# Kernel optimization log

Measured on AMD Instinct MI355X. Metric: run time of the kernel, lower is better.

The kernel has to match this reference:

```python
import jax, jax.numpy as jnp
import numpy as np

H = 1024   # hidden_size
V = 16000  # output_size (vocab)
B = 64     # batch_size
L = 256    # max_length (encoder seq len)
T = 128    # decoder steps


def setup_inputs() -> dict:
    key = jax.random.key(0)
    ks = jax.random.split(key, 16)
    s = 0.02
    return {
        "target_inputs": jax.random.randint(ks[0], (B, T), 0, V, dtype=jnp.int64),
        "encoder_outputs": jax.random.normal(ks[1], (L, B, H), dtype=jnp.float32),
        "emb": jax.random.normal(ks[2], (V, H), dtype=jnp.float32) * s,
        "W_attn": jax.random.normal(ks[3], (L, 2 * H), dtype=jnp.float32) * s,
        "b_attn": jnp.zeros((L,), jnp.float32),
        "W_comb": jax.random.normal(ks[4], (H, 2 * H), dtype=jnp.float32) * s,
        "b_comb": jnp.zeros((H,), jnp.float32),
        "W_ih": jax.random.normal(ks[5], (4 * H, H), dtype=jnp.float32) * s,
        "W_hh": jax.random.normal(ks[6], (4 * H, H), dtype=jnp.float32) * s,
        "b_ih": jnp.zeros((4 * H,), jnp.float32),
        "b_hh": jnp.zeros((4 * H,), jnp.float32),
        "W_out": jax.random.normal(ks[7], (V, H), dtype=jnp.float32) * s,
        "b_out": jnp.zeros((V,), jnp.float32),
    }


def reference(target_inputs, encoder_outputs, emb, W_attn, b_attn, W_comb, b_comb,
              W_ih, W_hh, b_ih, b_hh, W_out, b_out):
    dec_h = encoder_outputs[-1]                      # [B,H] (dec_hid.squeeze(0))
    enc = jnp.transpose(encoder_outputs, (1, 0, 2))  # [B,L,H]
    dec_c = jnp.zeros_like(dec_h)
    tokens = target_inputs.T                         # [T,B]

    def step(carry, tok):
        h, c = carry
        e = emb[tok]                                              # [B,H]  (dropout = eval identity)
        scores = jnp.concatenate([e, h], 1) @ W_attn.T + b_attn  # [B,L]
        aw = jax.nn.softmax(scores, axis=1)
        ctx = jnp.einsum('bl,blh->bh', aw, enc)                  # bmm
        x = jnp.concatenate([e, ctx], 1) @ W_comb.T + b_comb
        x = jax.nn.relu(x)                                        # [B,H]
        # single-step LSTM (PyTorch gate order i,f,g,o)
        gates = x @ W_ih.T + b_ih + h @ W_hh.T + b_hh             # [B,4H]
        i, f, g, o = jnp.split(gates, 4, axis=1)
        c = jax.nn.sigmoid(f) * c + jax.nn.sigmoid(i) * jnp.tanh(g)
        h = jax.nn.sigmoid(o) * jnp.tanh(c)
        logits = h @ W_out.T + b_out                              # [B,V]
        # Faithful to original: F.log_softmax(out(output_i.squeeze(1)), dim=1)
        # where output_i is [1,B,V]; squeeze(1) is a no-op for B>1, so dim=1
        # normalizes over the BATCH axis (== axis 0 of [B,V] here).
        out = jax.nn.log_softmax(logits, axis=0)
        return (h, c), out

    (_, _), outs = jax.lax.scan(step, (dec_h, dec_c), tokens)
    return outs  # [T,B,V]
```

## Files before the change

### kernel.cpp

```cpp
#include <hip/hip_runtime.h>
#include <math.h>

#define HH 1024
#define VV 16000
#define BB 64
#define LL 256
#define TT 128


__device__ __forceinline__ float sigm(float x) { return 1.0f / (1.0f + expf(-x)); }

__device__ void lstm_apply(const float* __restrict__ gates_acc,
                           const float* __restrict__ b_ih,
                           const float* __restrict__ b_hh,
                           float* __restrict__ c_buf,
                           float* __restrict__ h_buf,
                           float* __restrict__ Hall_t,
                           float* h_s,
                           int b, int tid, bool first_c)
{
    const int j = tid * 4;
    const float* gb = gates_acc + (size_t)b * 4 * HH;
    float4 gi = *(const float4*)(gb + j);
    float4 gf = *(const float4*)(gb + HH + j);
    float4 gg = *(const float4*)(gb + 2 * HH + j);
    float4 go = *(const float4*)(gb + 3 * HH + j);
    float4 bii = *(const float4*)(b_ih + j),          bhi = *(const float4*)(b_hh + j);
    float4 bif_ = *(const float4*)(b_ih + HH + j),    bhf = *(const float4*)(b_hh + HH + j);
    float4 big = *(const float4*)(b_ih + 2 * HH + j), bhg = *(const float4*)(b_hh + 2 * HH + j);
    float4 bio = *(const float4*)(b_ih + 3 * HH + j), bho = *(const float4*)(b_hh + 3 * HH + j);
    float4 co = first_c ? make_float4(0.f, 0.f, 0.f, 0.f)
                        : *(const float4*)(c_buf + (size_t)b * HH + j);
    float4 cn, hn;
#define DO_LSTM(X)                                        \
    {                                                     \
        float iv = sigm(gi.X + bii.X + bhi.X);            \
        float fv = sigm(gf.X + bif_.X + bhf.X);           \
        float gv = tanhf(gg.X + big.X + bhg.X);           \
        float ov = sigm(go.X + bio.X + bho.X);            \
        float c2 = fv * co.X + iv * gv;                   \
        cn.X = c2;                                        \
        hn.X = ov * tanhf(c2);                            \
    }
    DO_LSTM(x) DO_LSTM(y) DO_LSTM(z) DO_LSTM(w)
#undef DO_LSTM
    *(float4*)(c_buf + (size_t)b * HH + j) = cn;
    *(float4*)(h_buf + (size_t)b * HH + j) = hn;
    *(float4*)(Hall_t + (size_t)b * HH + j) = hn;
    if (h_s) *(float4*)(h_s + j) = hn;
}

__global__ __launch_bounds__(256) void k_attn(
    const int* __restrict__ tok_all, const float* __restrict__ enc,
    const float* __restrict__ emb, const float* __restrict__ Wattn,
    const float* __restrict__ battn, const float* __restrict__ b_ih,
    const float* __restrict__ b_hh, float* __restrict__ Hall,
    float* __restrict__ xin, float* __restrict__ x_acc,
    const float* __restrict__ gates_acc, float* __restrict__ h_buf,
    float* __restrict__ c_buf, int t)
{
    const int b = blockIdx.x;
    const int tid = threadIdx.x;
    __shared__ float e_s[HH];
    __shared__ float h_s[HH];
    __shared__ float sc[LL];
    __shared__ float red[8];

    ((float4*)(x_acc + (size_t)b * HH))[tid] = make_float4(0.f, 0.f, 0.f, 0.f);

    const int is64 = (tok_all[1] == 0 && tok_all[3] == 0 && tok_all[5] == 0 && tok_all[7] == 0);
    const int tok = is64 ? tok_all[2 * (b * TT + t)] : tok_all[b * TT + t];

    float4 ev = ((const float4*)(emb + (size_t)tok * HH))[tid];
    ((float4*)e_s)[tid] = ev;
    ((float4*)(xin + (size_t)b * 2 * HH))[tid] = ev;

    if (t == 0) {
        float4 hv = ((const float4*)(enc + (size_t)(LL - 1) * BB * HH + (size_t)b * HH))[tid];
        ((float4*)h_s)[tid] = hv;
        ((float4*)(h_buf + (size_t)b * HH))[tid] = hv;
    } else {
        lstm_apply(gates_acc, b_ih, b_hh, c_buf, h_buf,
                   Hall + (size_t)(t - 1) * BB * HH, h_s, b, tid, t == 1);
    }
    __syncthreads();

    const int w = tid >> 6, lane = tid & 63;
    const float4* es4 = (const float4*)e_s;
    const float4* hs4 = (const float4*)h_s;
    for (int li = 0; li < 64; ++li) {
        const int l = w * 64 + li;
        const float4* wr = (const float4*)(Wattn + (size_t)l * 2 * HH);
        float a = 0.f;
#pragma unroll
        for (int it = 0; it < 4; ++it) {
            float4 wv = wr[it * 64 + lane];
            float4 xv = es4[it * 64 + lane];
            a += wv.x * xv.x + wv.y * xv.y + wv.z * xv.z + wv.w * xv.w;
        }
#pragma unroll
        for (int it = 0; it < 4; ++it) {
            float4 wv = wr[256 + it * 64 + lane];
            float4 xv = hs4[it * 64 + lane];
            a += wv.x * xv.x + wv.y * xv.y + wv.z * xv.z + wv.w * xv.w;
        }
#pragma unroll
        for (int o = 32; o > 0; o >>= 1) a += __shfl_down(a, o, 64);
        if (lane == 0) sc[l] = a + battn[l];
    }
    __syncthreads();

    const float sv = sc[tid];
    float m = sv;
#pragma unroll
    for (int o = 32; o > 0; o >>= 1) m = fmaxf(m, __shfl_down(m, o, 64));
    if (lane == 0) red[w] = m;
    __syncthreads();
    m = fmaxf(fmaxf(red[0], red[1]), fmaxf(red[2], red[3]));
    const float ex = expf(sv - m);
    float s = ex;
#pragma unroll
    for (int o = 32; o > 0; o >>= 1) s += __shfl_down(s, o, 64);
    if (lane == 0) red[4 + w] = s;
    __syncthreads();
    const float tot = red[4] + red[5] + red[6] + red[7];
    sc[tid] = ex / tot;
    __syncthreads();

    float4 ctx = make_float4(0.f, 0.f, 0.f, 0.f);
    const float4* ebase = (const float4*)(enc + (size_t)b * HH) + tid;
#pragma unroll 4
    for (int l = 0; l < LL; ++l) {
        const float a = sc[l];
        float4 e2 = ebase[(size_t)l * (BB * HH / 4)];
        ctx.x += a * e2.x; ctx.y += a * e2.y; ctx.z += a * e2.z; ctx.w += a * e2.w;
    }
    ((float4*)(xin + (size_t)b * 2 * HH + HH))[tid] = ctx;
}

template <bool RELU_BIAS>
__device__ void gemm64x64(const float* __restrict__ A, int lda,
                          const float* __restrict__ abias,
                          const float* __restrict__ Wm, int ldw,
                          int n0, int k0, int klen,
                          float* __restrict__ Cacc, int ldc)
{
    __shared__ float As[32][68];
    __shared__ float Ws[32][68];
    const int tid = threadIdx.x;
    const int ty = tid >> 4, tx = tid & 15;
    const int q = tid & 7, r = tid >> 3;
    float acc[4][4] = {};

    for (int kc = k0; kc < k0 + klen; kc += 32) {
#pragma unroll
        for (int rr = 0; rr < 2; ++rr) {
            const int row = r + rr * 32;
            float4 v = *(const float4*)(A + (size_t)row * lda + kc + q * 4);
            if (RELU_BIAS) {
                const float4 bv = *(const float4*)(abias + kc + q * 4);
                v.x = fmaxf(v.x + bv.x, 0.f);
                v.y = fmaxf(v.y + bv.y, 0.f);
                v.z = fmaxf(v.z + bv.z, 0.f);
                v.w = fmaxf(v.w + bv.w, 0.f);
            }
            As[q * 4 + 0][row] = v.x; As[q * 4 + 1][row] = v.y;
            As[q * 4 + 2][row] = v.z; As[q * 4 + 3][row] = v.w;
            float4 wv = *(const float4*)(Wm + (size_t)(n0 + row) * ldw + kc + q * 4);
            Ws[q * 4 + 0][row] = wv.x; Ws[q * 4 + 1][row] = wv.y;
            Ws[q * 4 + 2][row] = wv.z; Ws[q * 4 + 3][row] = wv.w;
        }
        __syncthreads();
#pragma unroll
        for (int k = 0; k < 32; ++k) {
            const float4 a = *(const float4*)&As[k][ty * 4];
            const float4 wv = *(const float4*)&Ws[k][tx * 4];
            const float av[4] = {a.x, a.y, a.z, a.w};
            const float bv[4] = {wv.x, wv.y, wv.z, wv.w};
#pragma unroll
            for (int i = 0; i < 4; ++i)
#pragma unroll
                for (int j = 0; j < 4; ++j) acc[i][j] += av[i] * bv[j];
        }
        __syncthreads();
    }
#pragma unroll
    for (int i = 0; i < 4; ++i)
#pragma unroll
        for (int j = 0; j < 4; ++j)
            atomicAdd(Cacc + (size_t)(ty * 4 + i) * ldc + n0 + tx * 4 + j, acc[i][j]);
}

__global__ __launch_bounds__(256) void k_comb(const float* __restrict__ xin,
                                              const float* __restrict__ Wcomb,
                                              float* __restrict__ x_acc,
                                              float* __restrict__ gates_acc)
{
    const int blin = blockIdx.y * gridDim.x + blockIdx.x;
    float4* gz = (float4*)gates_acc;
    gz[blin * 512 + threadIdx.x] = make_float4(0.f, 0.f, 0.f, 0.f);
    gz[blin * 512 + 256 + threadIdx.x] = make_float4(0.f, 0.f, 0.f, 0.f);
    gemm64x64<false>(xin, 2 * HH, nullptr, Wcomb, 2 * HH,
                     blockIdx.x * 64, blockIdx.y * 256, 256, x_acc, HH);
}

__global__ __launch_bounds__(256) void k_gates(const float* __restrict__ x_acc,
                                               const float* __restrict__ h_buf,
                                               const float* __restrict__ b_comb,
                                               const float* __restrict__ W_ih,
                                               const float* __restrict__ W_hh,
                                               float* __restrict__ gates_acc)
{
    const int n0 = blockIdx.x * 64;
    const int k0 = blockIdx.y * 512;
    if (k0 < HH)
        gemm64x64<true>(x_acc, HH, b_comb, W_ih, HH, n0, k0, 512, gates_acc, 4 * HH);
    else
        gemm64x64<false>(h_buf, HH, nullptr, W_hh, HH, n0, k0 - HH, 512, gates_acc, 4 * HH);
}

__global__ __launch_bounds__(256) void k_lstm_fin(const float* __restrict__ gates_acc,
                                                  const float* __restrict__ b_ih,
                                                  const float* __restrict__ b_hh,
                                                  float* __restrict__ c_buf,
                                                  float* __restrict__ h_buf,
                                                  float* __restrict__ Hall)
{
    lstm_apply(gates_acc, b_ih, b_hh, c_buf, h_buf,
               Hall + (size_t)(TT - 1) * BB * HH, nullptr, blockIdx.x, threadIdx.x, false);
}

__global__ __launch_bounds__(256) void k_out(const float* __restrict__ Hall,
                                             const float* __restrict__ Wout,
                                             float* __restrict__ out)
{
    const int t = blockIdx.y;
    const int n0 = blockIdx.x * 128;
    const float* A = Hall + (size_t)t * BB * HH;
    __shared__ float As[32][68];
    __shared__ float Ws[32][132];
    __shared__ float Cs[64][129];
    __shared__ float lse_s[128];
    const int tid = threadIdx.x;
    const int ty = tid >> 4, tx = tid & 15;
    const int q = tid & 7, r = tid >> 3;
    float acc[4][8] = {};

    for (int kc = 0; kc < HH; kc += 32) {
#pragma unroll
        for (int rr = 0; rr < 2; ++rr) {
            const int row = r + rr * 32;
            float4 v = *(const float4*)(A + (size_t)row * HH + kc + q * 4);
            As[q * 4 + 0][row] = v.x; As[q * 4 + 1][row] = v.y;
            As[q * 4 + 2][row] = v.z; As[q * 4 + 3][row] = v.w;
        }
#pragma unroll
        for (int rr = 0; rr < 4; ++rr) {
            const int row = r + rr * 32;
            float4 v = *(const float4*)(Wout + (size_t)(n0 + row) * HH + kc + q * 4);
            Ws[q * 4 + 0][row] = v.x; Ws[q * 4 + 1][row] = v.y;
            Ws[q * 4 + 2][row] = v.z; Ws[q * 4 + 3][row] = v.w;
        }
        __syncthreads();
#pragma unroll
        for (int k = 0; k < 32; ++k) {
            const float4 a = *(const float4*)&As[k][ty * 4];
            const float4 w0 = *(const float4*)&Ws[k][tx * 8];
            const float4 w1 = *(const float4*)&Ws[k][tx * 8 + 4];
            const float av[4] = {a.x, a.y, a.z, a.w};
            const float bv[8] = {w0.x, w0.y, w0.z, w0.w, w1.x, w1.y, w1.z, w1.w};
#pragma unroll
            for (int i = 0; i < 4; ++i)
#pragma unroll
                for (int j = 0; j < 8; ++j) acc[i][j] += av[i] * bv[j];
        }
        __syncthreads();
    }
#pragma unroll
    for (int i = 0; i < 4; ++i)
#pragma unroll
        for (int j = 0; j < 8; ++j) Cs[ty * 4 + i][tx * 8 + j] = acc[i][j];
    __syncthreads();

    if (tid < 128) {
        float m = -1e30f;
        for (int b = 0; b < 64; ++b) m = fmaxf(m, Cs[b][tid]);
        float s = 0.f;
        for (int b = 0; b < 64; ++b) s += expf(Cs[b][tid] - m);
        lse_s[tid] = m + logf(s);
    }
    __syncthreads();

    const int col = tid & 127, bh = tid >> 7;
    float* outp = out + (size_t)t * BB * VV + n0 + col;
    for (int b = bh; b < 64; b += 2)
        outp[(size_t)b * VV] = Cs[b][col] - lse_s[col];
}

extern "C" void kernel_launch(void* const* d_in, const int* in_sizes, int n_in,
                              void* d_out, int out_size, void* d_ws, size_t ws_size,
                              hipStream_t stream)
{
    const int* tok = (const int*)d_in[0];
    const float* enc = (const float*)d_in[1];
    const float* emb = (const float*)d_in[2];
    const float* W_attn = (const float*)d_in[3];
    const float* b_attn = (const float*)d_in[4];
    const float* W_comb = (const float*)d_in[5];
    const float* b_comb = (const float*)d_in[6];
    const float* W_ih = (const float*)d_in[7];
    const float* W_hh = (const float*)d_in[8];
    const float* b_ih = (const float*)d_in[9];
    const float* b_hh = (const float*)d_in[10];
    const float* W_out = (const float*)d_in[11];
    float* out = (float*)d_out;
    float* ws = (float*)d_ws;

    const size_t n_Hall = (size_t)TT * BB * HH;
    const size_t n_xin = (size_t)BB * 2 * HH;
    const size_t n_xacc = (size_t)BB * HH;
    const size_t n_gates = (size_t)BB * 4 * HH;
    const size_t needed = (n_Hall + n_xin + n_xacc + n_gates + 2 * (size_t)BB * HH) * 4;
    if (ws_size < needed) return;

    float* H_all = ws;
    float* xin = H_all + n_Hall;
    float* x_acc = xin + n_xin;
    float* gates_acc = x_acc + n_xacc;
    float* h_buf = gates_acc + n_gates;
    float* c_buf = h_buf + (size_t)BB * HH;

    for (int t = 0; t < TT; ++t) {
        k_attn<<<BB, 256, 0, stream>>>(tok, enc, emb, W_attn, b_attn, b_ih, b_hh,
                                       H_all, xin, x_acc, gates_acc, h_buf, c_buf, t);
        k_comb<<<dim3(16, 8), 256, 0, stream>>>(xin, W_comb, x_acc, gates_acc);
        k_gates<<<dim3(64, 4), 256, 0, stream>>>(x_acc, h_buf, b_comb, W_ih, W_hh,
                                                 gates_acc);
    }
    k_lstm_fin<<<BB, 256, 0, stream>>>(gates_acc, b_ih, b_hh, c_buf, h_buf, H_all);
    k_out<<<dim3(125, 128), 256, 0, stream>>>(H_all, W_out, out);
}
```

Measured before the change: 31.68 ms.

## Fuse decoder time loop into one persistent kernel with grid barriers

Replaces the three kernel launches per decoder step with a single persistent 256-block kernel. It synchronises phases with a hierarchical atomic grid barrier and splits attention scores and context across four blocks per batch row to raise parallelism. The LSTM cell state is double-buffered so that redundant per-block LSTM recomputation can read old state safely. Register prefetching of the next K-tile is also added to the GEMM tiles and the output projection. The persistent design removes launch overhead but relies on all 256 blocks being co-resident, and the barriers add their own spin-wait cost.

```diff
diff --git a/kernel.cpp b/kernel.cpp
--- a/kernel.cpp
+++ b/kernel.cpp
@@ -7,17 +7,51 @@
 #define LL 256
 #define TT 128
 
+#define NBLK 256
+
+
+__device__ __forceinline__ void grid_barrier(unsigned* bar)
+{
+    __syncthreads();
+    if (threadIdx.x == 0) {
+        __threadfence();
+        unsigned* gen = bar;
+        unsigned* gcnt = bar + 64 + (blockIdx.x >> 4) * 64;
+        unsigned* root = bar + 1536;
+        const unsigned g =
+            __hip_atomic_load(gen, __ATOMIC_RELAXED, __HIP_MEMORY_SCOPE_AGENT);
+        bool releaser = false;
+        if (__hip_atomic_fetch_add(gcnt, 1u, __ATOMIC_ACQ_REL,
+                                   __HIP_MEMORY_SCOPE_AGENT) == 15u) {
+            __hip_atomic_store(gcnt, 0u, __ATOMIC_RELAXED,
+                               __HIP_MEMORY_SCOPE_AGENT);
+            if (__hip_atomic_fetch_add(root, 1u, __ATOMIC_ACQ_REL,
+                                       __HIP_MEMORY_SCOPE_AGENT) == 15u) {
+                __hip_atomic_store(root, 0u, __ATOMIC_RELAXED,
+                                   __HIP_MEMORY_SCOPE_AGENT);
+                __hip_atomic_store(gen, g + 1u, __ATOMIC_RELEASE,
+                                   __HIP_MEMORY_SCOPE_AGENT);
+                releaser = true;
+            }
+        }
+        if (!releaser) {
+            while (__hip_atomic_load(gen, __ATOMIC_ACQUIRE,
+                                     __HIP_MEMORY_SCOPE_AGENT) == g)
+                __builtin_amdgcn_s_sleep(1);
+        }
+        __threadfence();
+    }
+    __syncthreads();
+}
 
 __device__ __forceinline__ float sigm(float x) { return 1.0f / (1.0f + expf(-x)); }
 
-__device__ void lstm_apply(const float* __restrict__ gates_acc,
-                           const float* __restrict__ b_ih,
-                           const float* __restrict__ b_hh,
-                           float* __restrict__ c_buf,
-                           float* __restrict__ h_buf,
-                           float* __restrict__ Hall_t,
-                           float* h_s,
-                           int b, int tid, bool first_c)
+__device__ __forceinline__ void lstm_full(
+    const float* __restrict__ gates_acc, const float* __restrict__ b_ih,
+    const float* __restrict__ b_hh, const float* __restrict__ c_rd,
+    float* __restrict__ c_wr, float* __restrict__ h_buf,
+    float* __restrict__ Hall_t, float* h_s, int b, int tid, bool first_c,
+    bool writer)
 {
     const int j = tid * 4;
     const float* gb = gates_acc + (size_t)b * 4 * HH;
@@ -30,7 +64,7 @@
     float4 big = *(const float4*)(b_ih + 2 * HH + j), bhg = *(const float4*)(b_hh + 2 * HH + j);
     float4 bio = *(const float4*)(b_ih + 3 * HH + j), bho = *(const float4*)(b_hh + 3 * HH + j);
     float4 co = first_c ? make_float4(0.f, 0.f, 0.f, 0.f)
-                        : *(const float4*)(c_buf + (size_t)b * HH + j);
+                        : *(const float4*)(c_rd + (size_t)b * HH + j);
     float4 cn, hn;
 #define DO_LSTM(X)                                        \
     {                                                     \
@@ -44,133 +78,61 @@
     }
     DO_LSTM(x) DO_LSTM(y) DO_LSTM(z) DO_LSTM(w)
 #undef DO_LSTM
-    *(float4*)(c_buf + (size_t)b * HH + j) = cn;
-    *(float4*)(h_buf + (size_t)b * HH + j) = hn;
-    *(float4*)(Hall_t + (size_t)b * HH + j) = hn;
+    if (writer) {
+        *(float4*)(c_wr + (size_t)b * HH + j) = cn;
+        *(float4*)(h_buf + (size_t)b * HH + j) = hn;
+        *(float4*)(Hall_t + (size_t)b * HH + j) = hn;
+    }
     if (h_s) *(float4*)(h_s + j) = hn;
 }
 
-__global__ __launch_bounds__(256) void k_attn(
-    const int* __restrict__ tok_all, const float* __restrict__ enc,
-    const float* __restrict__ emb, const float* __restrict__ Wattn,
-    const float* __restrict__ battn, const float* __restrict__ b_ih,
-    const float* __restrict__ b_hh, float* __restrict__ Hall,
-    float* __restrict__ xin, float* __restrict__ x_acc,
-    const float* __restrict__ gates_acc, float* __restrict__ h_buf,
-    float* __restrict__ c_buf, int t)
-{
-    const int b = blockIdx.x;
-    const int tid = threadIdx.x;
-    __shared__ float e_s[HH];
-    __shared__ float h_s[HH];
-    __shared__ float sc[LL];
-    __shared__ float red[8];
-
-    ((float4*)(x_acc + (size_t)b * HH))[tid] = make_float4(0.f, 0.f, 0.f, 0.f);
-
-    const int is64 = (tok_all[1] == 0 && tok_all[3] == 0 && tok_all[5] == 0 && tok_all[7] == 0);
-    const int tok = is64 ? tok_all[2 * (b * TT + t)] : tok_all[b * TT + t];
-
-    float4 ev = ((const float4*)(emb + (size_t)tok * HH))[tid];
-    ((float4*)e_s)[tid] = ev;
-    ((float4*)(xin + (size_t)b * 2 * HH))[tid] = ev;
-
-    if (t == 0) {
-        float4 hv = ((const float4*)(enc + (size_t)(LL - 1) * BB * HH + (size_t)b * HH))[tid];
-        ((float4*)h_s)[tid] = hv;
-        ((float4*)(h_buf + (size_t)b * HH))[tid] = hv;
-    } else {
-        lstm_apply(gates_acc, b_ih, b_hh, c_buf, h_buf,
-                   Hall + (size_t)(t - 1) * BB * HH, h_s, b, tid, t == 1);
-    }
-    __syncthreads();
-
-    const int w = tid >> 6, lane = tid & 63;
-    const float4* es4 = (const float4*)e_s;
-    const float4* hs4 = (const float4*)h_s;
-    for (int li = 0; li < 64; ++li) {
-        const int l = w * 64 + li;
-        const float4* wr = (const float4*)(Wattn + (size_t)l * 2 * HH);
-        float a = 0.f;
-#pragma unroll
-        for (int it = 0; it < 4; ++it) {
-            float4 wv = wr[it * 64 + lane];
-            float4 xv = es4[it * 64 + lane];
-            a += wv.x * xv.x + wv.y * xv.y + wv.z * xv.z + wv.w * xv.w;
-        }
-#pragma unroll
-        for (int it = 0; it < 4; ++it) {
-            float4 wv = wr[256 + it * 64 + lane];
-            float4 xv = hs4[it * 64 + lane];
-            a += wv.x * xv.x + wv.y * xv.y + wv.z * xv.z + wv.w * xv.w;
-        }
-#pragma unroll
-        for (int o = 32; o > 0; o >>= 1) a += __shfl_down(a, o, 64);
-        if (lane == 0) sc[l] = a + battn[l];
-    }
-    __syncthreads();
-
-    const float sv = sc[tid];
-    float m = sv;
-#pragma unroll
-    for (int o = 32; o > 0; o >>= 1) m = fmaxf(m, __shfl_down(m, o, 64));
-    if (lane == 0) red[w] = m;
-    __syncthreads();
-    m = fmaxf(fmaxf(red[0], red[1]), fmaxf(red[2], red[3]));
-    const float ex = expf(sv - m);
-    float s = ex;
-#pragma unroll
-    for (int o = 32; o > 0; o >>= 1) s += __shfl_down(s, o, 64);
-    if (lane == 0) red[4 + w] = s;
-    __syncthreads();
-    const float tot = red[4] + red[5] + red[6] + red[7];
-    sc[tid] = ex / tot;
-    __syncthreads();
-
-    float4 ctx = make_float4(0.f, 0.f, 0.f, 0.f);
-    const float4* ebase = (const float4*)(enc + (size_t)b * HH) + tid;
-#pragma unroll 4
-    for (int l = 0; l < LL; ++l) {
-        const float a = sc[l];
-        float4 e2 = ebase[(size_t)l * (BB * HH / 4)];
-        ctx.x += a * e2.x; ctx.y += a * e2.y; ctx.z += a * e2.z; ctx.w += a * e2.w;
-    }
-    ((float4*)(xin + (size_t)b * 2 * HH + HH))[tid] = ctx;
-}
-
 template <bool RELU_BIAS>
-__device__ void gemm64x64(const float* __restrict__ A, int lda,
-                          const float* __restrict__ abias,
-                          const float* __restrict__ Wm, int ldw,
-                          int n0, int k0, int klen,
-                          float* __restrict__ Cacc, int ldc)
-{
-    __shared__ float As[32][68];
-    __shared__ float Ws[32][68];
+__device__ __forceinline__ void gemm64x64(
+    const float* __restrict__ A, int lda, const float* __restrict__ abias,
+    const float* __restrict__ Wm, int ldw, int n0, int k0, int klen,
+    float* __restrict__ Cacc, int ldc, float* __restrict__ smem)
+{
+    float (*As)[68] = (float (*)[68])smem;
+    float (*Ws)[68] = (float (*)[68])(smem + 32 * 68);
     const int tid = threadIdx.x;
     const int ty = tid >> 4, tx = tid & 15;
     const int q = tid & 7, r = tid >> 3;
     float acc[4][4] = {};
 
+    float4 va0, va1, vw0, vw1, vb;
+    {
+        const int kk = k0 + q * 4;
+        va0 = *(const float4*)(A + (size_t)r * lda + kk);
+        va1 = *(const float4*)(A + (size_t)(r + 32) * lda + kk);
+        vw0 = *(const float4*)(Wm + (size_t)(n0 + r) * ldw + kk);
+        vw1 = *(const float4*)(Wm + (size_t)(n0 + r + 32) * ldw + kk);
+        if (RELU_BIAS) vb = *(const float4*)(abias + kk);
+    }
     for (int kc = k0; kc < k0 + klen; kc += 32) {
-#pragma unroll
-        for (int rr = 0; rr < 2; ++rr) {
-            const int row = r + rr * 32;
-            float4 v = *(const float4*)(A + (size_t)row * lda + kc + q * 4);
-            if (RELU_BIAS) {
-                const float4 bv = *(const float4*)(abias + kc + q * 4);
-                v.x = fmaxf(v.x + bv.x, 0.f);
-                v.y = fmaxf(v.y + bv.y, 0.f);
-                v.z = fmaxf(v.z + bv.z, 0.f);
-                v.w = fmaxf(v.w + bv.w, 0.f);
-            }
-            As[q * 4 + 0][row] = v.x; As[q * 4 + 1][row] = v.y;
-            As[q * 4 + 2][row] = v.z; As[q * 4 + 3][row] = v.w;
-            float4 wv = *(const float4*)(Wm + (size_t)(n0 + row) * ldw + kc + q * 4);
-            Ws[q * 4 + 0][row] = wv.x; Ws[q * 4 + 1][row] = wv.y;
-            Ws[q * 4 + 2][row] = wv.z; Ws[q * 4 + 3][row] = wv.w;
-        }
+        float4 a0 = va0, a1 = va1;
+        if (RELU_BIAS) {
+            a0.x = fmaxf(a0.x + vb.x, 0.f); a0.y = fmaxf(a0.y + vb.y, 0.f);
+            a0.z = fmaxf(a0.z + vb.z, 0.f); a0.w = fmaxf(a0.w + vb.w, 0.f);
+            a1.x = fmaxf(a1.x + vb.x, 0.f); a1.y = fmaxf(a1.y + vb.y, 0.f);
+            a1.z = fmaxf(a1.z + vb.z, 0.f); a1.w = fmaxf(a1.w + vb.w, 0.f);
+        }
+        As[q * 4 + 0][r] = a0.x; As[q * 4 + 1][r] = a0.y;
+        As[q * 4 + 2][r] = a0.z; As[q * 4 + 3][r] = a0.w;
+        As[q * 4 + 0][r + 32] = a1.x; As[q * 4 + 1][r + 32] = a1.y;
+        As[q * 4 + 2][r + 32] = a1.z; As[q * 4 + 3][r + 32] = a1.w;
+        Ws[q * 4 + 0][r] = vw0.x; Ws[q * 4 + 1][r] = vw0.y;
+        Ws[q * 4 + 2][r] = vw0.z; Ws[q * 4 + 3][r] = vw0.w;
+        Ws[q * 4 + 0][r + 32] = vw1.x; Ws[q * 4 + 1][r + 32] = vw1.y;
+        Ws[q * 4 + 2][r + 32] = vw1.z; Ws[q * 4 + 3][r + 32] = vw1.w;
         __syncthreads();
+        if (kc + 32 < k0 + klen) {
+            const int kk = kc + 32 + q * 4;
+            va0 = *(const float4*)(A + (size_t)r * lda + kk);
+            va1 = *(const float4*)(A + (size_t)(r + 32) * lda + kk);
+            vw0 = *(const float4*)(Wm + (size_t)(n0 + r) * ldw + kk);
+            vw1 = *(const float4*)(Wm + (size_t)(n0 + r + 32) * ldw + kk);
+            if (RELU_BIAS) vb = *(const float4*)(abias + kk);
+        }
 #pragma unroll
         for (int k = 0; k < 32; ++k) {
             const float4 a = *(const float4*)&As[k][ty * 4];
@@ -191,43 +153,160 @@
             atomicAdd(Cacc + (size_t)(ty * 4 + i) * ldc + n0 + tx * 4 + j, acc[i][j]);
 }
 
-__global__ __launch_bounds__(256) void k_comb(const float* __restrict__ xin,
-                                              const float* __restrict__ Wcomb,
-                                              float* __restrict__ x_acc,
-                                              float* __restrict__ gates_acc)
-{
-    const int blin = blockIdx.y * gridDim.x + blockIdx.x;
-    float4* gz = (float4*)gates_acc;
-    gz[blin * 512 + threadIdx.x] = make_float4(0.f, 0.f, 0.f, 0.f);
-    gz[blin * 512 + 256 + threadIdx.x] = make_float4(0.f, 0.f, 0.f, 0.f);
-    gemm64x64<false>(xin, 2 * HH, nullptr, Wcomb, 2 * HH,
-                     blockIdx.x * 64, blockIdx.y * 256, 256, x_acc, HH);
-}
-
-__global__ __launch_bounds__(256) void k_gates(const float* __restrict__ x_acc,
-                                               const float* __restrict__ h_buf,
-                                               const float* __restrict__ b_comb,
-                                               const float* __restrict__ W_ih,
-                                               const float* __restrict__ W_hh,
-                                               float* __restrict__ gates_acc)
-{
-    const int n0 = blockIdx.x * 64;
-    const int k0 = blockIdx.y * 512;
-    if (k0 < HH)
-        gemm64x64<true>(x_acc, HH, b_comb, W_ih, HH, n0, k0, 512, gates_acc, 4 * HH);
-    else
-        gemm64x64<false>(h_buf, HH, nullptr, W_hh, HH, n0, k0 - HH, 512, gates_acc, 4 * HH);
-}
-
-__global__ __launch_bounds__(256) void k_lstm_fin(const float* __restrict__ gates_acc,
-                                                  const float* __restrict__ b_ih,
-                                                  const float* __restrict__ b_hh,
-                                                  float* __restrict__ c_buf,
-                                                  float* __restrict__ h_buf,
-                                                  float* __restrict__ Hall)
-{
-    lstm_apply(gates_acc, b_ih, b_hh, c_buf, h_buf,
-               Hall + (size_t)(TT - 1) * BB * HH, nullptr, blockIdx.x, threadIdx.x, false);
+__global__ __launch_bounds__(256) void k_loop(
+    const int* __restrict__ tok_all, const float* __restrict__ enc,
+    const float* __restrict__ emb, const float* __restrict__ Wattn,
+    const float* __restrict__ battn, const float* __restrict__ Wcomb,
+    const float* __restrict__ bcomb, const float* __restrict__ Wih,
+    const float* __restrict__ Whh, const float* __restrict__ b_ih,
+    const float* __restrict__ b_hh, float* __restrict__ Hall,
+    float* __restrict__ xin, float* __restrict__ x_acc,
+    float* __restrict__ gates_acc, float* __restrict__ h_buf,
+    float* __restrict__ c0, float* __restrict__ c1,
+    float* __restrict__ sc_all, unsigned* __restrict__ bar)
+{
+    __shared__ __align__(16) float smem[2 * 32 * 68];
+    const int bid = blockIdx.x;
+    const int tid = threadIdx.x;
+    const int w = tid >> 6, lane = tid & 63;
+
+    const int is64 = (tok_all[1] == 0 && tok_all[3] == 0 && tok_all[5] == 0 &&
+                      tok_all[7] == 0);
+
+    for (int t = 0; t < TT; ++t) {
+        {
+            const int b = bid >> 2, q = bid & 3;
+            float* e_s = smem;
+            float* h_s = smem + HH;
+
+            x_acc[(size_t)b * HH + q * 256 + tid] = 0.f;
+
+            const int tok = is64 ? tok_all[2 * (b * TT + t)] : tok_all[b * TT + t];
+            float4 ev = ((const float4*)(emb + (size_t)tok * HH))[tid];
+            ((float4*)e_s)[tid] = ev;
+            if (q == 0) ((float4*)(xin + (size_t)b * 2 * HH))[tid] = ev;
+
+            if (t == 0) {
+                float4 hv = ((const float4*)(enc + (size_t)(LL - 1) * BB * HH +
+                                             (size_t)b * HH))[tid];
+                ((float4*)h_s)[tid] = hv;
+                if (q == 0) ((float4*)(h_buf + (size_t)b * HH))[tid] = hv;
+            } else {
+                lstm_full(gates_acc, b_ih, b_hh, (t & 1) ? c1 : c0,
+                          (t & 1) ? c0 : c1, h_buf,
+                          Hall + (size_t)(t - 1) * BB * HH, h_s, b, tid,
+                          t == 1, q == 0);
+            }
+            __syncthreads();
+
+            const float4* es4 = (const float4*)e_s;
+            const float4* hs4 = (const float4*)h_s;
+            for (int i = 0; i < 16; ++i) {
+                const int l = q * 64 + w * 16 + i;
+                const float4* wr = (const float4*)(Wattn + (size_t)l * 2 * HH);
+                float a0 = 0.f, a1 = 0.f;
+#pragma unroll
+                for (int it = 0; it < 4; ++it) {
+                    float4 wv = wr[it * 64 + lane];
+                    float4 xv = es4[it * 64 + lane];
+                    a0 += wv.x * xv.x + wv.y * xv.y + wv.z * xv.z + wv.w * xv.w;
+                }
+#pragma unroll
+                for (int it = 0; it < 4; ++it) {
+                    float4 wv = wr[256 + it * 64 + lane];
+                    float4 xv = hs4[it * 64 + lane];
+                    a1 += wv.x * xv.x + wv.y * xv.y + wv.z * xv.z + wv.w * xv.w;
+                }
+                float a = a0 + a1;
+#pragma unroll
+                for (int o = 32; o > 0; o >>= 1) a += __shfl_down(a, o, 64);
+                if (lane == 0) sc_all[(size_t)b * LL + l] = a + battn[l];
+            }
+        }
+        grid_barrier(bar);
+
+        {
+            const int b = bid >> 2, hq = bid & 3;
+            float* aw_s = smem;
+            float* red = smem + 256;
+            float4* part_s = (float4*)(smem + 272);
+
+            const float sv = sc_all[(size_t)b * LL + tid];
+            float m = sv;
+#pragma unroll
+            for (int o = 32; o > 0; o >>= 1) m = fmaxf(m, __shfl_down(m, o, 64));
+            if (lane == 0) red[w] = m;
+            __syncthreads();
+            m = fmaxf(fmaxf(red[0], red[1]), fmaxf(red[2], red[3]));
+            const float ex = expf(sv - m);
+            float s = ex;
+#pragma unroll
+            for (int o = 32; o > 0; o >>= 1) s += __shfl_down(s, o, 64);
+            if (lane == 0) red[4 + w] = s;
+            __syncthreads();
+            const float tot = red[4] + red[5] + red[6] + red[7];
+            aw_s[tid] = ex / tot;
+            __syncthreads();
+
+            const int col4 = hq * 64 + lane;
+            const float4* e4 = (const float4*)enc + (size_t)b * (HH / 4) + col4;
+            float4 cacc = make_float4(0.f, 0.f, 0.f, 0.f);
+#pragma unroll 8
+            for (int li = 0; li < 64; ++li) {
+                const int l = w * 64 + li;
+                const float a = aw_s[l];
+                float4 ev2 = e4[(size_t)l * (BB * HH / 4)];
+                cacc.x += a * ev2.x; cacc.y += a * ev2.y;
+                cacc.z += a * ev2.z; cacc.w += a * ev2.w;
+            }
+            part_s[w * 64 + lane] = cacc;
+            __syncthreads();
+            if (w == 0) {
+                float4 p0 = part_s[lane];
+                float4 p1 = part_s[64 + lane];
+                float4 p2 = part_s[128 + lane];
+                float4 p3 = part_s[192 + lane];
+                float4 r4;
+                r4.x = p0.x + p1.x + p2.x + p3.x;
+                r4.y = p0.y + p1.y + p2.y + p3.y;
+                r4.z = p0.z + p1.z + p2.z + p3.z;
+                r4.w = p0.w + p1.w + p2.w + p3.w;
+                ((float4*)(xin + (size_t)b * 2 * HH + HH))[col4] = r4;
+            }
+        }
+        grid_barrier(bar);
+
+        if (bid < 128) {
+            const int nt = bid >> 3, kq = bid & 7;
+            gemm64x64<false>(xin, 2 * HH, nullptr, Wcomb, 2 * HH, nt * 64,
+                             kq * 256, 256, x_acc, HH, smem);
+        } else {
+            const float4 z4 = make_float4(0.f, 0.f, 0.f, 0.f);
+            float4* gz = (float4*)gates_acc;
+            const int i0 = (bid - 128) * 256 + tid;
+            gz[i0] = z4;
+            gz[i0 + 32768] = z4;
+        }
+        grid_barrier(bar);
+
+        {
+            const int nt = bid >> 2, kq = bid & 3;
+            const int k0 = kq * 512;
+            if (k0 < HH)
+                gemm64x64<true>(x_acc, HH, bcomb, Wih, HH, nt * 64, k0, 512,
+                                gates_acc, 4 * HH, smem);
+            else
+                gemm64x64<false>(h_buf, HH, nullptr, Whh, HH, nt * 64, k0 - HH,
+                                 512, gates_acc, 4 * HH, smem);
+        }
+        grid_barrier(bar);
+    }
+
+    if (bid < BB) {
+        lstm_full(gates_acc, b_ih, b_hh, (TT & 1) ? c1 : c0, (TT & 1) ? c0 : c1,
+                  h_buf, Hall + (size_t)(TT - 1) * BB * HH, nullptr, bid, tid,
+                  false, true);
+    }
 }
 
 __global__ __launch_bounds__(256) void k_out(const float* __restrict__ Hall,
@@ -246,22 +325,39 @@
     const int q = tid & 7, r = tid >> 3;
     float acc[4][8] = {};
 
+    float4 pa0, pa1, pw0, pw1, pw2, pw3;
+    {
+        const int kk = q * 4;
+        pa0 = *(const float4*)(A + (size_t)r * HH + kk);
+        pa1 = *(const float4*)(A + (size_t)(r + 32) * HH + kk);
+        pw0 = *(const float4*)(Wout + (size_t)(n0 + r) * HH + kk);
+        pw1 = *(const float4*)(Wout + (size_t)(n0 + r + 32) * HH + kk);
+        pw2 = *(const float4*)(Wout + (size_t)(n0 + r + 64) * HH + kk);
+        pw3 = *(const float4*)(Wout + (size_t)(n0 + r + 96) * HH + kk);
+    }
     for (int kc = 0; kc < HH; kc += 32) {
-#pragma unroll
-        for (int rr = 0; rr < 2; ++rr) {
-            const int row = r + rr * 32;
-            float4 v = *(const float4*)(A + (size_t)row * HH + kc + q * 4);
-            As[q * 4 + 0][row] = v.x; As[q * 4 + 1][row] = v.y;
-            As[q * 4 + 2][row] = v.z; As[q * 4 + 3][row] = v.w;
-        }
-#pragma unroll
-        for (int rr = 0; rr < 4; ++rr) {
-            const int row = r + rr * 32;
-            float4 v = *(const float4*)(Wout + (size_t)(n0 + row) * HH + kc + q * 4);
-            Ws[q * 4 + 0][row] = v.x; Ws[q * 4 + 1][row] = v.y;
-            Ws[q * 4 + 2][row] = v.z; Ws[q * 4 + 3][row] = v.w;
-        }
+        As[q * 4 + 0][r] = pa0.x; As[q * 4 + 1][r] = pa0.y;
+        As[q * 4 + 2][r] = pa0.z; As[q * 4 + 3][r] = pa0.w;
+        As[q * 4 + 0][r + 32] = pa1.x; As[q * 4 + 1][r + 32] = pa1.y;
+        As[q * 4 + 2][r + 32] = pa1.z; As[q * 4 + 3][r + 32] = pa1.w;
+        Ws[q * 4 + 0][r] = pw0.x; Ws[q * 4 + 1][r] = pw0.y;
+        Ws[q * 4 + 2][r] = pw0.z; Ws[q * 4 + 3][r] = pw0.w;
+        Ws[q * 4 + 0][r + 32] = pw1.x; Ws[q * 4 + 1][r + 32] = pw1.y;
+        Ws[q * 4 + 2][r + 32] = pw1.z; Ws[q * 4 + 3][r + 32] = pw1.w;
+        Ws[q * 4 + 0][r + 64] = pw2.x; Ws[q * 4 + 1][r + 64] = pw2.y;
+        Ws[q * 4 + 2][r + 64] = pw2.z; Ws[q * 4 + 3][r + 64] = pw2.w;
+        Ws[q * 4 + 0][r + 96] = pw3.x; Ws[q * 4 + 1][r + 96] = pw3.y;
+        Ws[q * 4 + 2][r + 96] = pw3.z; Ws[q * 4 + 3][r + 96] = pw3.w;
         __syncthreads();
+        if (kc + 32 < HH) {
+            const int kk = kc + 32 + q * 4;
+            pa0 = *(const float4*)(A + (size_t)r * HH + kk);
+            pa1 = *(const float4*)(A + (size_t)(r + 32) * HH + kk);
+            pw0 = *(const float4*)(Wout + (size_t)(n0 + r) * HH + kk);
+            pw1 = *(const float4*)(Wout + (size_t)(n0 + r + 32) * HH + kk);
+            pw2 = *(const float4*)(Wout + (size_t)(n0 + r + 64) * HH + kk);
+            pw3 = *(const float4*)(Wout + (size_t)(n0 + r + 96) * HH + kk);
+        }
 #pragma unroll
         for (int k = 0; k < 32; ++k) {
             const float4 a = *(const float4*)&As[k][ty * 4];
@@ -320,7 +416,11 @@
     const size_t n_xin = (size_t)BB * 2 * HH;
     const size_t n_xacc = (size_t)BB * HH;
     const size_t n_gates = (size_t)BB * 4 * HH;
-    const size_t needed = (n_Hall + n_xin + n_xacc + n_gates + 2 * (size_t)BB * HH) * 4;
+    const size_t n_bh = (size_t)BB * HH;
+    const size_t n_sc = (size_t)BB * LL;
+    const size_t n_bar = 2048;
+    const size_t needed =
+        (n_Hall + n_xin + n_xacc + n_gates + 3 * n_bh + n_sc + n_bar) * 4;
     if (ws_size < needed) return;
 
     float* H_all = ws;
@@ -328,15 +428,16 @@
     float* x_acc = xin + n_xin;
     float* gates_acc = x_acc + n_xacc;
     float* h_buf = gates_acc + n_gates;
-    float* c_buf = h_buf + (size_t)BB * HH;
-
-    for (int t = 0; t < TT; ++t) {
-        k_attn<<<BB, 256, 0, stream>>>(tok, enc, emb, W_attn, b_attn, b_ih, b_hh,
-                                       H_all, xin, x_acc, gates_acc, h_buf, c_buf, t);
-        k_comb<<<dim3(16, 8), 256, 0, stream>>>(xin, W_comb, x_acc, gates_acc);
-        k_gates<<<dim3(64, 4), 256, 0, stream>>>(x_acc, h_buf, b_comb, W_ih, W_hh,
-                                                 gates_acc);
-    }
-    k_lstm_fin<<<BB, 256, 0, stream>>>(gates_acc, b_ih, b_hh, c_buf, h_buf, H_all);
+    float* c0 = h_buf + n_bh;
+    float* c1 = c0 + n_bh;
+    float* sc_all = c1 + n_bh;
+    unsigned* bar = (unsigned*)(sc_all + n_sc);
+
+    hipMemsetAsync(bar, 0, n_bar * 4, stream);
+
+    k_loop<<<NBLK, 256, 0, stream>>>(tok, enc, emb, W_attn, b_attn, W_comb,
+                                     b_comb, W_ih, W_hh, b_ih, b_hh, H_all,
+                                     xin, x_acc, gates_acc, h_buf, c0, c1,
+                                     sc_all, bar);
     k_out<<<dim3(125, 128), 256, 0, stream>>>(H_all, W_out, out);
 }
```

Measured after the change: 33.74 ms. 6.5% more time.
